# Kernel optimization log

Measured on AMD Instinct MI355X. Metric: run time of the kernel, lower is better.

Reference implementation:

```python
import jax, jax.numpy as jnp
import numpy as np

NEG = -1e9  # stands in for -inf in masked_fill; identical softmax output, grad-safe


def _sfu(inputs, fusion, Wr, Wg):
    # SFU: m = [x, f, x*f, x-f]; o = relu(m@Wr)*g + (1-g)*x, g = sigmoid(m@Wg)
    m = jnp.concatenate([inputs, fusion, inputs * fusion, inputs - fusion], axis=-1)
    x = jax.nn.relu(m @ Wr)
    g = jax.nn.sigmoid(m @ Wg)
    return x * g + (1.0 - g) * inputs


def _stage(U, V, cmask, qmask, E, B, p):
    # One Aligner stage = InterAlign followed by SelfAlign. Batch-first layout (b, len, d).
    Wu, bu, Wv, bv, Wri, Wgi, gi, W1, b1, W2, b2, Wrs, Wgs, gs = p
    # ---- InterAlign ----
    Ct = jax.nn.relu(U @ Wu + bu)              # (b, c, d)
    Qt = jax.nn.relu(V @ Wv + bv)              # (b, q, d)
    E0 = jnp.einsum('bcd,bqd->bcq', Ct, Qt)    # (b, c, q)
    if E is not None:
        Es = jax.nn.softmax(jnp.where(cmask[:, :, None] == 0, NEG, E), axis=1)   # softmax over c
        Bs = jax.nn.softmax(jnp.where(cmask[:, None, :] == 0, NEG, B), axis=2)   # softmax over c (cols)
        E = E0 + gi * jnp.einsum('bce,beq->bcq', Bs, Es)
    else:
        E = E0
    Ett = jax.nn.softmax(jnp.where(qmask[:, None, :] == 0, NEG, E), axis=2)
    qctx = jnp.einsum('bcq,bqd->bcd', Ett, V)  # attend question
    h = _sfu(U, qctx, Wri, Wgi)
    # ---- SelfAlign ----
    H1 = jax.nn.relu(h @ W1 + b1)
    H2 = jax.nn.relu(h @ W2 + b2)
    B0 = jnp.einsum('bcd,bed->bce', H1, H2)    # (b, c, c)
    if B is not None:
        B1s = jax.nn.softmax(jnp.where(cmask[:, :, None] == 0, NEG, B), axis=1)
        B2s = jax.nn.softmax(jnp.where(cmask[:, None, :] == 0, NEG, B), axis=2)
        B = B0 + gs * jnp.einsum('bce,bef->bcf', B2s, B1s)
    else:
        B = B0
    c = U.shape[1]
    B = B * (1.0 - jnp.eye(c, dtype=B.dtype))[None]  # masked_fill_(eye, 0.0): zero diagonal
    Btt = jax.nn.softmax(jnp.where(cmask[:, None, :] == 0, NEG, B), axis=2)
    hctx = jnp.einsum('bce,bed->bcd', Btt, h)
    Z = _sfu(h, hctx, Wrs, Wgs)
    return Z, E, B


def setup_inputs() -> dict:
    key = jax.random.key(0)
    b, c_len, q_len, d = 8, 768, 96, 768
    T = 2  # number of aligner stages
    ks = jax.random.split(key, 16)
    s = 0.02
    inp = {
        'U': jax.random.normal(ks[0], (b, c_len, d), jnp.float32),
        'V': jax.random.normal(ks[1], (b, q_len, d), jnp.float32),
        'U_mask': jax.random.randint(ks[2], (b, c_len), 0, 2).astype(jnp.int32),
        'V_mask': jax.random.randint(ks[3], (b, q_len), 0, 2).astype(jnp.int32),
        'Wu': jax.random.normal(ks[4], (T, d, d), jnp.float32) * s,
        'bu': jnp.zeros((T, d), jnp.float32),
        'Wv': jax.random.normal(ks[5], (T, d, d), jnp.float32) * s,
        'bv': jnp.zeros((T, d), jnp.float32),
        'Wr_i': jax.random.normal(ks[6], (T, 4 * d, d), jnp.float32) * s,
        'Wg_i': jax.random.normal(ks[7], (T, 4 * d, d), jnp.float32) * s,
        'gamma_i': jnp.full((T,), 3.0, jnp.float32),
        'W1': jax.random.normal(ks[8], (T, d, d), jnp.float32) * s,
        'b1': jnp.zeros((T, d), jnp.float32),
        'W2': jax.random.normal(ks[9], (T, d, d), jnp.float32) * s,
        'b2': jnp.zeros((T, d), jnp.float32),
        'Wr_s': jax.random.normal(ks[10], (T, 4 * d, d), jnp.float32) * s,
        'Wg_s': jax.random.normal(ks[11], (T, 4 * d, d), jnp.float32) * s,
        'gamma_s': jnp.full((T,), 3.0, jnp.float32),
    }
    return inp


def reference(U, V, U_mask, V_mask, Wu, bu, Wv, bv, Wr_i, Wg_i, gamma_i,
              W1, b1, W2, b2, Wr_s, Wg_s, gamma_s):
    E = None
    B = None
    x = U
    for t in range(Wu.shape[0]):  # fixed small stage loop (align_1 -> align_2)
        p = (Wu[t], bu[t], Wv[t], bv[t], Wr_i[t], Wg_i[t], gamma_i[t],
             W1[t], b1[t], W2[t], b2[t], Wr_s[t], Wg_s[t], gamma_s[t])
        x, E, B = _stage(x, V, U_mask, V_mask, E, B, p)
    return x
```

## Files before the change

### kernel.cpp

```cpp
#include <hip/hip_runtime.h>
#include <math.h>

#define NEGV -1e9f

typedef short bf16x8 __attribute__((ext_vector_type(8)));
typedef float f32x4 __attribute__((ext_vector_type(4)));
typedef unsigned short ushort8v __attribute__((ext_vector_type(8)));

static __device__ __forceinline__ unsigned short f2bf(float f) {
  unsigned int u = __float_as_uint(f);
  unsigned int r = (u + 0x7fffu + ((u >> 16) & 1u)) >> 16;
  return (unsigned short)r;
}

static __device__ __forceinline__ int xcd_swz(int lin, int nwg) {
  int q = nwg >> 3, r = nwg & 7;
  int x = lin & 7, i = lin >> 3;
  return (x < r) ? x * (q + 1) + i : r * (q + 1) + (x - r) * q + i;
}

__device__ __forceinline__ float wred_max(float v) {
  #pragma unroll
  for (int o = 32; o > 0; o >>= 1) v = fmaxf(v, __shfl_down(v, o, 64));
  return v;
}
__device__ __forceinline__ float wred_sum(float v) {
  #pragma unroll
  for (int o = 32; o > 0; o >>= 1) v += __shfl_down(v, o, 64);
  return v;
}

__global__ __launch_bounds__(256)
void softmax_row_mask(const float* __restrict__ X, const int* __restrict__ mask,
                      float* __restrict__ Y, unsigned short* __restrict__ Ybf,
                      int R, int Cn)
{
  int bz = blockIdx.y, r = blockIdx.x, tid = threadIdx.x;
  const float* xr = X + ((size_t)bz * R + r) * Cn;
  const int*   mr = mask + (size_t)bz * Cn;
  float*       yr = Y ? (Y + ((size_t)bz * R + r) * Cn) : nullptr;
  unsigned short* yb = Ybf ? (Ybf + ((size_t)bz * R + r) * Cn) : nullptr;
  __shared__ float sred[4];

  float mx = -INFINITY;
  for (int i = tid; i < Cn; i += 256) {
    float v = (mr[i] != 0) ? xr[i] : NEGV;
    mx = fmaxf(mx, v);
  }
  float wm = wred_max(mx);
  if ((tid & 63) == 0) sred[tid >> 6] = wm;
  __syncthreads();
  mx = fmaxf(fmaxf(sred[0], sred[1]), fmaxf(sred[2], sred[3]));
  __syncthreads();

  float s = 0.f;
  for (int i = tid; i < Cn; i += 256) {
    float v = (mr[i] != 0) ? xr[i] : NEGV;
    s += expf(v - mx);
  }
  float wsv = wred_sum(s);
  if ((tid & 63) == 0) sred[tid >> 6] = wsv;
  __syncthreads();
  s = sred[0] + sred[1] + sred[2] + sred[3];
  float inv = 1.0f / s;

// ... 143 lines not shown
  int tr = t >> 4, tc4 = (t & 15) * 4;
  #pragma unroll
  for (int rr = 0; rr < 4; ++rr) {
    int r = tr + rr * 16;
    ushort4 v = *reinterpret_cast<const ushort4*>(X + (size_t)(r0 + r) * 768 + c0 + tc4);
    T[r][tc4 + 0] = v.x; T[r][tc4 + 1] = v.y;
    T[r][tc4 + 2] = v.z; T[r][tc4 + 3] = v.w;
  }
  __syncthreads();
  #pragma unroll
  for (int rr = 0; rr < 4; ++rr) {
    int cc = tr + rr * 16;
    ushort4 o;
    o.x = T[tc4 + 0][cc]; o.y = T[tc4 + 1][cc];
    o.z = T[tc4 + 2][cc]; o.w = T[tc4 + 3][cc];
    *reinterpret_cast<ushort4*>(Y + (size_t)(c0 + cc) * 768 + r0 + tc4) = o;
  }
}

__global__ __launch_bounds__(256)
void transpV(const float* __restrict__ V, unsigned short* __restrict__ VT)
{
  int bz = blockIdx.z;
  const float* Vb = V + (size_t)bz * 96 * 768;
  unsigned short* Yb = VT + (size_t)bz * 768 * 96;
  __shared__ float T[64][65];
  int c0 = blockIdx.x * 64, r0 = blockIdx.y * 64;
  int t = threadIdx.x;
  int tr = t >> 4, tc4 = (t & 15) * 4;
  #pragma unroll
  for (int rr = 0; rr < 4; ++rr) {
    int r = tr + rr * 16;
    int gr = r0 + r;
    float4 v = make_float4(0.f, 0.f, 0.f, 0.f);
    if (gr < 96)
      v = *reinterpret_cast<const float4*>(Vb + (size_t)gr * 768 + c0 + tc4);
    T[r][tc4 + 0] = v.x; T[r][tc4 + 1] = v.y;
    T[r][tc4 + 2] = v.z; T[r][tc4 + 3] = v.w;
  }
  __syncthreads();
  #pragma unroll
  for (int rr = 0; rr < 4; ++rr) {
    int cc = tr + rr * 16;
    int gc = c0 + cc;
    #pragma unroll
    for (int e = 0; e < 4; ++e) {
      int gr = r0 + tc4 + e;
      if (gr < 96) Yb[(size_t)gc * 96 + gr] = f2bf(T[tc4 + e][cc]);
    }
  }
}

__global__ __launch_bounds__(256)
void transp_cast4(const float* __restrict__ W0, const float* __restrict__ W1a,
                  const float* __restrict__ W2a, const float* __restrict__ W3a,
                  unsigned short* __restrict__ Wt)
{
  int z = blockIdx.z;
  const float* W = (z == 0) ? W0 : (z == 1) ? W1a : (z == 2) ? W2a : W3a;
  unsigned short* Y = Wt + (size_t)z * 768 * 768;
  __shared__ float T[64][65];
  int n0 = blockIdx.x * 64, k0 = blockIdx.y * 64;
  int t = threadIdx.x;
  int tr = t >> 4, tc4 = (t & 15) * 4;
  #pragma unroll
  for (int r = 0; r < 4; ++r) {
    int k = tr + r * 16;
    float4 v = *reinterpret_cast<const float4*>(W + (size_t)(k0 + k) * 768 + n0 + tc4);
    T[k][tc4 + 0] = v.x; T[k][tc4 + 1] = v.y; T[k][tc4 + 2] = v.z; T[k][tc4 + 3] = v.w;
  }
  __syncthreads();
  #pragma unroll
  for (int r = 0; r < 4; ++r) {
    int n = tr + r * 16;
    ushort4 o;
    o.x = f2bf(T[tc4 + 0][n]); o.y = f2bf(T[tc4 + 1][n]);
    o.z = f2bf(T[tc4 + 2][n]); o.w = f2bf(T[tc4 + 3][n]);
    *reinterpret_cast<ushort4*>(Y + (size_t)(n0 + n) * 768 + k0 + tc4) = o;
  }
}

__global__ __launch_bounds__(256)
void transp_cast2x4(const float* __restrict__ W0, const float* __restrict__ W1a,
                    const float* __restrict__ W2a, const float* __restrict__ W3a,
                    unsigned short* __restrict__ Wt)
{
  int z = blockIdx.z;
  const float* W = (z == 0) ? W0 : (z == 1) ? W1a : (z == 2) ? W2a : W3a;
  unsigned short* Y = Wt + (size_t)z * 768 * 2304;
  __shared__ float T[64][65];
  int n0 = blockIdx.x * 64, k0 = blockIdx.y * 64;
  int t = threadIdx.x;
  int tr = t >> 4, tc4 = (t & 15) * 4;
  #pragma unroll
  for (int r = 0; r < 4; ++r) {
    int k = tr + r * 16;
    int gk = k0 + k;
    float4 v = *reinterpret_cast<const float4*>(W + (size_t)gk * 768 + n0 + tc4);
    if (gk < 768) {
      float4 u = *reinterpret_cast<const float4*>(W + (size_t)(gk + 2304) * 768 + n0 + tc4);
      v.x += u.x; v.y += u.y; v.z += u.z; v.w += u.w;
    } else if (gk < 1536) {
      float4 u = *reinterpret_cast<const float4*>(W + (size_t)(gk + 1536) * 768 + n0 + tc4);
      v.x -= u.x; v.y -= u.y; v.z -= u.z; v.w -= u.w;
    }
    T[k][tc4 + 0] = v.x; T[k][tc4 + 1] = v.y; T[k][tc4 + 2] = v.z; T[k][tc4 + 3] = v.w;
  }
  __syncthreads();
  #pragma unroll
  for (int r = 0; r < 4; ++r) {
    int n = tr + r * 16;
    ushort4 o;
    o.x = f2bf(T[tc4 + 0][n]); o.y = f2bf(T[tc4 + 1][n]);
    o.z = f2bf(T[tc4 + 2][n]); o.w = f2bf(T[tc4 + 3][n]);
    *reinterpret_cast<ushort4*>(Y + (size_t)(n0 + n) * 2304 + k0 + tc4) = o;
  }
}

__global__ __launch_bounds__(256)
void cast_bf16(const float* __restrict__ X, unsigned short* __restrict__ Y, int n8)
{
  int idx = blockIdx.x * 256 + threadIdx.x;
  if (idx >= n8) return;
  float4 a0 = *reinterpret_cast<const float4*>(X + (size_t)idx * 8);
  float4 a1 = *reinterpret_cast<const float4*>(X + (size_t)idx * 8 + 4);
  ushort8v o;
  o[0] = f2bf(a0.x); o[1] = f2bf(a0.y); o[2] = f2bf(a0.z); o[3] = f2bf(a0.w);
  o[4] = f2bf(a1.x); o[5] = f2bf(a1.y); o[6] = f2bf(a1.z); o[7] = f2bf(a1.w);
  *reinterpret_cast<ushort8v*>(Y + (size_t)idx * 8) = o;
}


template<int NB, int WAVES>
__global__ __launch_bounds__(64 * WAVES)
void mfma_gemm(const unsigned short* __restrict__ A,
               const unsigned short* __restrict__ Bt0,
               const unsigned short* __restrict__ Bt1,
               const float* __restrict__ bias0, const float* __restrict__ bias1,
               const float* __restrict__ alphap, const float* __restrict__ C0,
               float* __restrict__ F0, float* __restrict__ F1,
               unsigned short* __restrict__ O0, unsigned short* __restrict__ O1,
               int M, int N, int K,
               long sA, long sB, long sC0, long sC,
               int relu, int zerodiag,
               const float* __restrict__ Xc, unsigned short* __restrict__ McO)
{
  const int RG = WAVES / 4;
  const int TM = RG * 48;
  __shared__ unsigned short As[2][TM * 32];
  __shared__ unsigned short Bs0[2][2048];
  __shared__ unsigned short Bs1[2][NB == 2 ? 2048 : 16];

  int nx = gridDim.x, ny = gridDim.y;
  int nwg = nx * ny * gridDim.z;
  int lin = blockIdx.x + nx * (blockIdx.y + ny * blockIdx.z);
  int sw = xcd_swz(lin, nwg);
  int bxi = sw % nx; int rest = sw / nx;
  int byi = rest % ny; int bz = rest / ny;

  A   += (size_t)bz * sA;
  Bt0 += (size_t)bz * sB;
  if (NB == 2) Bt1 += (size_t)bz * sB;
  const float* C0b = C0 ? (C0 + (size_t)bz * sC0) : nullptr;

  int tid = threadIdx.x;
  int w = tid >> 6, l = tid & 63;
  int m0 = byi * TM, n0 = bxi * 64;
  int wr = w >> 2, wc = w & 3;

  int g8 = (((l & 3) ^ ((l >> 3) & 3))) * 8;
  int rowA = w * 16 + (l >> 2); if (rowA > TM - 1) rowA = TM - 1;
  int rB = n0 + (w & 3) * 16 + (l >> 2); if (rB > N - 1) rB = N - 1;
  const unsigned short* srcA  = A + (size_t)(m0 + rowA) * K + g8;
  const unsigned short* srcB0 = Bt0 + (size_t)rB * K + g8;
  const unsigned short* srcB1 = (NB == 2) ? Bt1 + (size_t)rB * K + g8 : nullptr;

#define GG_STAGE(kt, bi) do { int kk0 = (kt) * 32;                                                                        \
    if (w < TM / 16)                                                                                                      \
      __builtin_amdgcn_global_load_lds((const unsigned int*)(srcA + kk0),  (unsigned int*)&As[bi][0]  + w * 256, 16, 0, 0); \
    if (w < 4)                                                                                                            \
      __builtin_amdgcn_global_load_lds((const unsigned int*)(srcB0 + kk0), (unsigned int*)&Bs0[bi][0] + w * 256, 16, 0, 0); \
    if (NB == 2 && w >= 4)                                                                                                \
      __builtin_amdgcn_global_load_lds((const unsigned int*)(srcB1 + kk0), (unsigned int*)&Bs1[bi][0] + (w - 4) * 256, 16, 0, 0); \
  } while (0)

  f32x4 a0[3] = {};
  f32x4 a1v[3] = {};

  const int NT = K / 32;
  int prm = ((l >> 4) ^ ((l >> 1) & 3)) * 8;
  GG_STAGE(0, 0);
  __syncthreads();
  int cur = 0;
  for (int kt = 0; kt < NT; ++kt) {
    if (kt + 1 < NT) GG_STAGE(kt + 1, cur ^ 1);

    bf16x8 af[3];
    #pragma unroll
    for (int i = 0; i < 3; ++i) {
      int off = (wr * 48 + i * 16 + (l & 15)) * 32 + prm;
      af[i] = *reinterpret_cast<const bf16x8*>(&As[cur][off]);
    }
    int offB = (wc * 16 + (l & 15)) * 32 + prm;
    bf16x8 b0 = *reinterpret_cast<const bf16x8*>(&Bs0[cur][offB]);
    #pragma unroll
    for (int i = 0; i < 3; ++i)
      a0[i] = __builtin_amdgcn_mfma_f32_16x16x32_bf16(af[i], b0, a0[i], 0, 0, 0);
    if (NB == 2) {
      bf16x8 b1 = *reinterpret_cast<const bf16x8*>(&Bs1[cur][offB]);
      #pragma unroll
      for (int i = 0; i < 3; ++i)
        a1v[i] = __builtin_amdgcn_mfma_f32_16x16x32_bf16(af[i], b1, a1v[i], 0, 0, 0);
    }
    __syncthreads();
    cur ^= 1;
  }
#undef GG_STAGE

  float alpha = alphap ? alphap[0] : 1.0f;
  float* F0b = F0 ? F0 + (size_t)bz * sC : nullptr;
  float* F1b = F1 ? F1 + (size_t)bz * sC : nullptr;
  unsigned short* O0b = O0 ? O0 + (size_t)bz * sC : nullptr;
  unsigned short* O1b = O1 ? O1 + (size_t)bz * sC : nullptr;
  const float* Xcb = Xc ? Xc + (size_t)bz * 589824 : nullptr;
  unsigned short* Mcb = McO ? McO + (size_t)bz * 1769472 : nullptr;

  #pragma unroll
  for (int i = 0; i < 3; ++i) {
    #pragma unroll
    for (int qq = 0; qq < 4; ++qq) {
      int gm = m0 + wr * 48 + i * 16 + (l >> 4) * 4 + qq;
      int gn = n0 + wc * 16 + (l & 15);
      if (gn >= N) continue;
      size_t oidx = (size_t)gm * N + gn;
      float v = alpha * a0[i][qq];
      if (bias0) v += bias0[gn];
      if (relu) v = fmaxf(v, 0.f);
      if (C0b) v += C0b[oidx];
      if (zerodiag && gm == gn) v = 0.f;
      if (Mcb) {
        float xv = Xcb[(size_t)gm * 768 + gn];
        size_t mrow = (size_t)gm * 2304 + gn;
        Mcb[mrow]        = f2bf(xv);
        Mcb[mrow + 768]  = f2bf(v);
        Mcb[mrow + 1536] = f2bf(xv * v);
      }
      if (F0b) F0b[oidx] = v;
      if (O0b) O0b[oidx] = f2bf(v);
      if (NB == 2) {
        float v1 = alpha * a1v[i][qq];
        if (bias1) v1 += bias1[gn];
        if (relu) v1 = fmaxf(v1, 0.f);
        if (F1b) F1b[oidx] = v1;
        if (O1b) O1b[oidx] = f2bf(v1);
      }
    }
  }
}

__global__ __launch_bounds__(512)
void mfma_relu_pair(const unsigned short* __restrict__ A1g,
                    const unsigned short* __restrict__ B1g,
                    const float* __restrict__ bias1g, unsigned short* __restrict__ O1g,
                    const unsigned short* __restrict__ A2g,
                    const unsigned short* __restrict__ B2g,
                    const float* __restrict__ bias2g, unsigned short* __restrict__ O2g)
{
  const int K = 768, N = 768, NT = 24;
  __shared__ unsigned short As[2][3072];
  __shared__ unsigned short Bs0[2][2048];

  int nx = gridDim.x, ny = gridDim.y;
  int nwg = nx * ny;
  int lin = blockIdx.x + nx * blockIdx.y;
  int sw = xcd_swz(lin, nwg);
  int bxi = sw % nx; int byi = sw / nx;

  const unsigned short* A; const unsigned short* Bt;
  const float* bias; unsigned short* O;
  int m0;
  if (byi < 64) { A = A1g; Bt = B1g; bias = bias1g; O = O1g; m0 = byi * 96; }
  else          { A = A2g; Bt = B2g; bias = bias2g; O = O2g; m0 = (byi - 64) * 96; }

  int tid = threadIdx.x;
  int w = tid >> 6, l = tid & 63;
  int n0 = bxi * 64;
  int wr = w >> 2, wc = w & 3;

  int g8 = (((l & 3) ^ ((l >> 3) & 3))) * 8;
  int rowA = w * 16 + (l >> 2); if (rowA > 95) rowA = 95;
  int rB = n0 + (w & 3) * 16 + (l >> 2);
  const unsigned short* srcA  = A + (size_t)(m0 + rowA) * K + g8;
  const unsigned short* srcB0 = Bt + (size_t)rB * K + g8;

#define RP_STAGE(kt, bi) do { int kk0 = (kt) * 32;                                                                        \
    if (w < 6)                                                                                                            \
      __builtin_amdgcn_global_load_lds((const unsigned int*)(srcA + kk0),  (unsigned int*)&As[bi][0]  + w * 256, 16, 0, 0); \
    if (w < 4)                                                                                                            \
      __builtin_amdgcn_global_load_lds((const unsigned int*)(srcB0 + kk0), (unsigned int*)&Bs0[bi][0] + w * 256, 16, 0, 0); \
  } while (0)

  f32x4 a0[3] = {};
  int prm = ((l >> 4) ^ ((l >> 1) & 3)) * 8;
  RP_STAGE(0, 0);
  __syncthreads();
  int cur = 0;
  for (int kt = 0; kt < NT; ++kt) {
    if (kt + 1 < NT) RP_STAGE(kt + 1, cur ^ 1);

    bf16x8 af[3];
    #pragma unroll
    for (int i = 0; i < 3; ++i) {
      int off = (wr * 48 + i * 16 + (l & 15)) * 32 + prm;
      af[i] = *reinterpret_cast<const bf16x8*>(&As[cur][off]);
    }
    int offB = (wc * 16 + (l & 15)) * 32 + prm;
    bf16x8 b0 = *reinterpret_cast<const bf16x8*>(&Bs0[cur][offB]);
    #pragma unroll
    for (int i = 0; i < 3; ++i)
      a0[i] = __builtin_amdgcn_mfma_f32_16x16x32_bf16(af[i], b0, a0[i], 0, 0, 0);
    __syncthreads();
    cur ^= 1;
  }
#undef RP_STAGE

  #pragma unroll
  for (int i = 0; i < 3; ++i) {
    #pragma unroll
    for (int qq = 0; qq < 4; ++qq) {
      int gm = m0 + wr * 48 + i * 16 + (l >> 4) * 4 + qq;
      int gn = n0 + wc * 16 + (l & 15);
      float v = a0[i][qq] + bias[gn];
      v = fmaxf(v, 0.f);
      O[(size_t)gm * N + gn] = f2bf(v);
    }
  }
}

__global__ __launch_bounds__(512)
void qctx_fused(const float* __restrict__ E, const int* __restrict__ Vm,
                const unsigned short* __restrict__ VTb,
                const float* __restrict__ X, unsigned short* __restrict__ Mc)
{
  __shared__ unsigned short As3[3][3072];
  __shared__ unsigned short Bs3[3][2048];
  __shared__ int mk[96];

  int nx = gridDim.x, ny = gridDim.y;
  int nwg = nx * ny * gridDim.z;
  int lin = blockIdx.x + nx * (blockIdx.y + ny * blockIdx.z);
  int sw = xcd_swz(lin, nwg);
  int bxi = sw % nx; int rest = sw / nx;
  int byi = rest % ny; int bz = rest / ny;

  int tid = threadIdx.x;
  int w = tid >> 6, l = tid & 63;
  int m0 = byi * 96, n0 = bxi * 64;

  int g8 = (((l & 3) ^ ((l >> 3) & 3))) * 8;
  if (w < 4) {
    int rB = n0 + w * 16 + (l >> 2);
    const unsigned short* srcB = VTb + ((size_t)bz * 768 + rB) * 96 + g8;
    #pragma unroll
    for (int kt = 0; kt < 3; ++kt)
      __builtin_amdgcn_global_load_lds((const unsigned int*)(srcB + kt * 32),
                                       (unsigned int*)&Bs3[kt][0] + w * 256, 16, 0, 0);
  }
  if (tid < 96) mk[tid] = Vm[bz * 96 + tid];
  __syncthreads();

  if (tid < 384) {
    int r = tid >> 2, j4 = tid & 3;
    const float* er = E + ((size_t)bz * 768 + m0 + r) * 96 + j4 * 24;
    float va[24];
    #pragma unroll
    for (int u = 0; u < 6; ++u) {
      float4 v = *reinterpret_cast<const float4*>(er + u * 4);
      int kb = j4 * 24 + u * 4;
      va[u * 4 + 0] = mk[kb + 0] ? v.x : NEGV;
      va[u * 4 + 1] = mk[kb + 1] ? v.y : NEGV;
      va[u * 4 + 2] = mk[kb + 2] ? v.z : NEGV;
      va[u * 4 + 3] = mk[kb + 3] ? v.w : NEGV;
    }
    float mx = -INFINITY;
    #pragma unroll
    for (int u = 0; u < 24; ++u) mx = fmaxf(mx, va[u]);
    mx = fmaxf(mx, __shfl_xor(mx, 1, 64));
    mx = fmaxf(mx, __shfl_xor(mx, 2, 64));
    float s = 0.f;
    #pragma unroll
    for (int u = 0; u < 24; ++u) { va[u] = expf(va[u] - mx); s += va[u]; }
    s += __shfl_xor(s, 1, 64);
    s += __shfl_xor(s, 2, 64);
    float inv = 1.0f / s;
    #pragma unroll
    for (int g = 0; g < 3; ++g) {
      int gG = j4 * 3 + g;
      int kt = gG >> 2, Gin = gG & 3;
      ushort8v o;
      #pragma unroll
      for (int e = 0; e < 8; ++e) o[e] = f2bf(va[g * 8 + e] * inv);
      int idx = (r >> 4) * 512 + ((r & 15) * 4 + (Gin ^ ((r >> 1) & 3))) * 8;
      *reinterpret_cast<ushort8v*>(&As3[kt][idx]) = o;
    }
  }
  __syncthreads();

  int wr = w >> 2, wc = w & 3;
  int prm = ((l >> 4) ^ ((l >> 1) & 3)) * 8;
  f32x4 acc[3] = {};
  #pragma unroll
  for (int kt = 0; kt < 3; ++kt) {
    bf16x8 af[3];
    #pragma unroll
    for (int i = 0; i < 3; ++i) {
      int off = (wr * 48 + i * 16 + (l & 15)) * 32 + prm;
      af[i] = *reinterpret_cast<const bf16x8*>(&As3[kt][off]);
    }
    int offB = (wc * 16 + (l & 15)) * 32 + prm;
    bf16x8 b0 = *reinterpret_cast<const bf16x8*>(&Bs3[kt][offB]);
    #pragma unroll
    for (int i = 0; i < 3; ++i)
      acc[i] = __builtin_amdgcn_mfma_f32_16x16x32_bf16(af[i], b0, acc[i], 0, 0, 0);
  }

  const float* Xb = X + (size_t)bz * 589824;
  unsigned short* Mcb = Mc + (size_t)bz * 1769472;
  #pragma unroll
  for (int i = 0; i < 3; ++i) {
    #pragma unroll
    for (int qq = 0; qq < 4; ++qq) {
      int gm = m0 + wr * 48 + i * 16 + (l >> 4) * 4 + qq;
      int gn = n0 + wc * 16 + (l & 15);
      float v = acc[i][qq];
      float xv = Xb[(size_t)gm * 768 + gn];
      size_t mrow = (size_t)gm * 2304 + gn;
      Mcb[mrow]        = f2bf(xv);
      Mcb[mrow + 768]  = f2bf(v);
      Mcb[mrow + 1536] = f2bf(xv * v);
    }
  }
}

__global__ __launch_bounds__(512)
void mfma_dual2(const unsigned short* __restrict__ A1,
                const unsigned short* __restrict__ B1t,
                const unsigned short* __restrict__ A2,
                const unsigned short* __restrict__ B2t,
                const float* __restrict__ alphap, float* __restrict__ F0,
                int M, int N, int K,
                long sA1, long sB1, long sA2, long sB2, long sC,
                int zerodiag)
{
  __shared__ unsigned short As1[2][3072], Bs1[2][2048];
  __shared__ unsigned short As2[2][3072], Bs2[2][2048];

  int nx = gridDim.x, ny = gridDim.y;
  int nwg = nx * ny * gridDim.z;
  int lin = blockIdx.x + nx * (blockIdx.y + ny * blockIdx.z);
  int sw = xcd_swz(lin, nwg);
  int bxi = sw % nx; int rest = sw / nx;
  int byi = rest % ny; int bz = rest / ny;

  A1  += (size_t)bz * sA1;
  B1t += (size_t)bz * sB1;
  A2  += (size_t)bz * sA2;
  B2t += (size_t)bz * sB2;

  int tid = threadIdx.x;
  int w = tid >> 6, l = tid & 63;
  int m0 = byi * 96, n0 = bxi * 64;
  int wr = w >> 2, wc = w & 3;

  int g8 = (((l & 3) ^ ((l >> 3) & 3))) * 8;
  int rowA = w * 16 + (l >> 2); if (rowA > 95) rowA = 95;
  int rB = n0 + (w & 3) * 16 + (l >> 2);
  const unsigned short* srcA1 = A1 + (size_t)(m0 + rowA) * K + g8;
  const unsigned short* srcA2 = A2 + (size_t)(m0 + rowA) * K + g8;
  const unsigned short* srcB1 = B1t + (size_t)rB * K + g8;
  const unsigned short* srcB2 = B2t + (size_t)rB * K + g8;

#define D2_STAGE(kt, bi) do { int kk0 = (kt) * 32;                                                                        \
    if (w < 6) {                                                                                                          \
      __builtin_amdgcn_global_load_lds((const unsigned int*)(srcA1 + kk0), (unsigned int*)&As1[bi][0] + w * 256, 16, 0, 0); \
      __builtin_amdgcn_global_load_lds((const unsigned int*)(srcA2 + kk0), (unsigned int*)&As2[bi][0] + w * 256, 16, 0, 0); \
    }                                                                                                                     \
    if (w < 4)                                                                                                            \
      __builtin_amdgcn_global_load_lds((const unsigned int*)(srcB1 + kk0), (unsigned int*)&Bs1[bi][0] + w * 256, 16, 0, 0); \
    else                                                                                                                  \
      __builtin_amdgcn_global_load_lds((const unsigned int*)(srcB2 + kk0), (unsigned int*)&Bs2[bi][0] + (w - 4) * 256, 16, 0, 0); \
  } while (0)

  f32x4 ac1[3] = {};
  f32x4 ac2[3] = {};

  const int NT = K / 32;
  int prm = ((l >> 4) ^ ((l >> 1) & 3)) * 8;
  D2_STAGE(0, 0);
  __syncthreads();
  int cur = 0;
  for (int kt = 0; kt < NT; ++kt) {
    if (kt + 1 < NT) D2_STAGE(kt + 1, cur ^ 1);

    int offB = (wc * 16 + (l & 15)) * 32 + prm;
    bf16x8 af1[3], af2[3];
    #pragma unroll
    for (int i = 0; i < 3; ++i) {
      int off = (wr * 48 + i * 16 + (l & 15)) * 32 + prm;
      af1[i] = *reinterpret_cast<const bf16x8*>(&As1[cur][off]);
      af2[i] = *reinterpret_cast<const bf16x8*>(&As2[cur][off]);
    }
    bf16x8 b1 = *reinterpret_cast<const bf16x8*>(&Bs1[cur][offB]);
    bf16x8 b2 = *reinterpret_cast<const bf16x8*>(&Bs2[cur][offB]);
    #pragma unroll
    for (int i = 0; i < 3; ++i) {
      ac1[i] = __builtin_amdgcn_mfma_f32_16x16x32_bf16(af1[i], b1, ac1[i], 0, 0, 0);
      ac2[i] = __builtin_amdgcn_mfma_f32_16x16x32_bf16(af2[i], b2, ac2[i], 0, 0, 0);
    }
    __syncthreads();
    cur ^= 1;
  }
#undef D2_STAGE

  float alpha = alphap[0];
  float* F0b = F0 + (size_t)bz * sC;
  #pragma unroll
  for (int i = 0; i < 3; ++i) {
    #pragma unroll
    for (int qq = 0; qq < 4; ++qq) {
      int gm = m0 + wr * 48 + i * 16 + (l >> 4) * 4 + qq;
      int gn = n0 + wc * 16 + (l & 15);
      float v = ac1[i][qq] + alpha * ac2[i][qq];
      if (zerodiag && gm == gn) v = 0.f;
      F0b[(size_t)gm * N + gn] = v;
    }
  }
}

__global__ __launch_bounds__(512)
void sfu_mfma(const unsigned short* __restrict__ Mc,
              const unsigned short* __restrict__ Brt,
              const unsigned short* __restrict__ Bgt,
              const float* __restrict__ Xres, float* __restrict__ Z,
              unsigned short* __restrict__ Zb)
{
  __shared__ unsigned short As[2][3072];
  __shared__ unsigned short Brs[2][2048];
  __shared__ unsigned short Bgs[2][2048];
  const int K = 2304;
  const int NT = 72;

  int nx = gridDim.x, ny = gridDim.y;
  int nwg = nx * ny;
  int lin = blockIdx.x + nx * blockIdx.y;
  int sw = xcd_swz(lin, nwg);
  int bxi = sw % nx; int byi = sw / nx;

  int tid = threadIdx.x;
  int w = tid >> 6, l = tid & 63;
  int m0 = byi * 96, n0 = bxi * 64;
  int wr = w >> 2, wc = w & 3;

  int g8 = (((l & 3) ^ ((l >> 3) & 3))) * 8;
  int rowA = w * 16 + (l >> 2); if (rowA > 95) rowA = 95;
  int rB = n0 + (w & 3) * 16 + (l >> 2);
  const unsigned short* srcA = Mc  + (size_t)(m0 + rowA) * K + g8;
  const unsigned short* srcR = Brt + (size_t)rB * K + g8;
  const unsigned short* srcG = Bgt + (size_t)rB * K + g8;

#define SFU_STAGE(kt, bi) do { int kk0 = (kt) * 32;                                                                      \
    if (w < 6)                                                                                                           \
      __builtin_amdgcn_global_load_lds((const unsigned int*)(srcA + kk0), (unsigned int*)&As[bi][0]  + w * 256, 16, 0, 0); \
    if (w < 4)                                                                                                           \
      __builtin_amdgcn_global_load_lds((const unsigned int*)(srcR + kk0), (unsigned int*)&Brs[bi][0] + w * 256, 16, 0, 0); \
    if (w >= 4)                                                                                                          \
      __builtin_amdgcn_global_load_lds((const unsigned int*)(srcG + kk0), (unsigned int*)&Bgs[bi][0] + (w - 4) * 256, 16, 0, 0); \
  } while (0)

  f32x4 aR[3] = {};
  f32x4 aG[3] = {};

  int prm = ((l >> 4) ^ ((l >> 1) & 3)) * 8;
  SFU_STAGE(0, 0);
  __syncthreads();
  int cur = 0;
  for (int kt = 0; kt < NT; ++kt) {
    if (kt + 1 < NT) SFU_STAGE(kt + 1, cur ^ 1);

    bf16x8 af[3];
    #pragma unroll
    for (int i = 0; i < 3; ++i) {
      int off = (wr * 48 + i * 16 + (l & 15)) * 32 + prm;
      af[i] = *reinterpret_cast<const bf16x8*>(&As[cur][off]);
    }
    int offB = (wc * 16 + (l & 15)) * 32 + prm;
    bf16x8 br = *reinterpret_cast<const bf16x8*>(&Brs[cur][offB]);
    bf16x8 bg = *reinterpret_cast<const bf16x8*>(&Bgs[cur][offB]);
    #pragma unroll
    for (int i = 0; i < 3; ++i) {
      aR[i] = __builtin_amdgcn_mfma_f32_16x16x32_bf16(af[i], br, aR[i], 0, 0, 0);
      aG[i] = __builtin_amdgcn_mfma_f32_16x16x32_bf16(af[i], bg, aG[i], 0, 0, 0);
    }
    __syncthreads();
    cur ^= 1;
  }
#undef SFU_STAGE

  #pragma unroll
  for (int i = 0; i < 3; ++i) {
    #pragma unroll
    for (int qq = 0; qq < 4; ++qq) {
      int gm = m0 + wr * 48 + i * 16 + (l >> 4) * 4 + qq;
      int gn = n0 + wc * 16 + (l & 15);
      float r = fmaxf(aR[i][qq], 0.f);
      float g = 1.0f / (1.0f + expf(-aG[i][qq]));
      float xv = Xres[(size_t)gm * 768 + gn];
      float z = r * g + (1.0f - g) * xv;
      Z[(size_t)gm * 768 + gn] = z;
      if (Zb) Zb[(size_t)gm * 768 + gn] = f2bf(z);
    }
  }
}

static void launch_mfma1(const unsigned short* A, const unsigned short* Bt,
                         const float* bias, const float* alphap, const float* C0,
                         float* F0, unsigned short* O0,
                         int M, int N, int K, long sA, long sB, long sC0, long sC,
                         int relu, int zd, int batch, int tm, hipStream_t s,
                         const float* xcat = nullptr, unsigned short* mco = nullptr)
{
  dim3 g((N + 63) / 64, M / tm, batch);
  if (tm == 48)
    mfma_gemm<1, 4><<<g, 256, 0, s>>>(A, Bt, nullptr, bias, nullptr, alphap, C0,
                                      F0, nullptr, O0, nullptr, M, N, K, sA, sB, sC0, sC, relu, zd,
                                      xcat, mco);
  else
    mfma_gemm<1, 8><<<g, 512, 0, s>>>(A, Bt, nullptr, bias, nullptr, alphap, C0,
                                      F0, nullptr, O0, nullptr, M, N, K, sA, sB, sC0, sC, relu, zd,
                                      xcat, mco);
}

static void launch_mfma2(const unsigned short* A, const unsigned short* Bt0,
                         const unsigned short* Bt1, const float* bias0, const float* bias1,
                         unsigned short* O0, unsigned short* O1,
                         int M, int N, int K, long sA, long sB,
                         int relu, int batch, hipStream_t s)
{
  dim3 g((N + 63) / 64, M / 96, batch);
  mfma_gemm<2, 8><<<g, 512, 0, s>>>(A, Bt0, Bt1, bias0, bias1, nullptr, nullptr,
                                    nullptr, nullptr, O0, O1, M, N, K, sA, sB, 0, sA,
                                    relu, 0, nullptr, nullptr);
}

extern "C" void kernel_launch(void* const* d_in, const int* in_sizes, int n_in,
                              void* d_out, int out_size, void* d_ws, size_t ws_size,
                              hipStream_t stream)
{
  const int b = 8, c = 768, q = 96, d = 768, T = 2;
  const float* U   = (const float*)d_in[0];
  const float* V   = (const float*)d_in[1];
  const int*   Um  = (const int*)d_in[2];
  const int*   Vm  = (const int*)d_in[3];
  const float* Wu  = (const float*)d_in[4];
  const float* bu  = (const float*)d_in[5];
  const float* Wv  = (const float*)d_in[6];
  const float* bv  = (const float*)d_in[7];
  const float* Wri = (const float*)d_in[8];
  const float* Wgi = (const float*)d_in[9];
  const float* gi  = (const float*)d_in[10];
  const float* W1  = (const float*)d_in[11];
  const float* b1  = (const float*)d_in[12];
  const float* W2  = (const float*)d_in[13];
  const float* b2  = (const float*)d_in[14];
  const float* Wrs = (const float*)d_in[15];
  const float* Wgs = (const float*)d_in[16];
  const float* gs  = (const float*)d_in[17];
  float* out = (float*)d_out;

  const size_t big = (size_t)b * c * d;
  const size_t smE = (size_t)b * c * q;
  float* ws   = (float*)d_ws;
  float* xbuf = ws + 0 * big;
  float* h    = ws + 1 * big;
  float* Bm   = ws + 2 * big;
  float* t1   = ws + 3 * big;
  float* t2   = ws + 4 * big;
  float* t3   = ws + 5 * big;
  float* t4   = ws + 6 * big;
  float* Ebuf = ws + 7 * big;
  float* E0b  = Ebuf + smE;
  float* Esb  = E0b + smE;
  float* spare = Esb + smE;
  float* slotE = spare + smE;
  float* WTf  = slotE + big / 2;

  unsigned short* Mc  = (unsigned short*)t1;
  unsigned short* Wt  = (unsigned short*)t4;
  unsigned short* t1h = (unsigned short*)t1;
  unsigned short* t3h = (unsigned short*)t3;
  unsigned short* t3h2 = t3h + big;
  unsigned short* slotEb = (unsigned short*)slotE;
  unsigned short* H1b = t1h;
  unsigned short* H2b = H1b + big;
  float* SMst = spare;
  float* SSst = spare + 73728;
  unsigned short* WuT = (unsigned short*)WTf;
  unsigned short* WvT  = WuT  + (size_t)d * d;
  unsigned short* W1T  = WvT  + (size_t)d * d;
  unsigned short* W2T  = W1T  + (size_t)d * d;
  unsigned short* Vb16 = W2T  + (size_t)d * d;
  unsigned short* Qtbb = Vb16 + smE;
  unsigned short* VTb  = Qtbb + smE;
  unsigned short* EsTb = VTb  + smE;

  const long cd = (long)c * d, cq = (long)c * q, qd = (long)q * d, cc = (long)c * c;
  const size_t dd = (size_t)d * d;
  const size_t wslice = (size_t)768 * 2304;
  const int cast_big = (int)(big / 8);
  (void)ws_size;

  const float* x = U;
  for (int t = 0; t < T; ++t) {
    const float* Writ = Wri + (size_t)t * 4 * dd;
    const float* Wgit = Wgi + (size_t)t * 4 * dd;
    const float* Wrst = Wrs + (size_t)t * 4 * dd;
    const float* Wgst = Wgs + (size_t)t * 4 * dd;

    transp_cast4<<<dim3(12, 12, 4), 256, 0, stream>>>(Wu + t * dd, Wv + t * dd,
                                                      W1 + t * dd, W2 + t * dd, WuT);
    transp_cast2x4<<<dim3(12, 36, 4), 256, 0, stream>>>(Writ, Wgit, Wrst, Wgst, Wt);
    if (t == 0) {
      cast_bf16<<<dim3((int)(smE / 8 / 256)), 256, 0, stream>>>(V, Vb16, (int)(smE / 8));
      transpV<<<dim3(12, 2, b), 256, 0, stream>>>(V, VTb);
      cast_bf16<<<dim3(cast_big / 256), 256, 0, stream>>>(x, t3h, cast_big);
    }

    mfma_relu_pair<<<dim3(12, 72), 512, 0, stream>>>(t3h, WuT, bu + t * d, t1h,
                                                     Vb16, WvT, bv + t * d, Qtbb);
    float* e0dst = (t == 0) ? Ebuf : E0b;
    launch_mfma1(t1h, Qtbb, nullptr, nullptr, nullptr, e0dst, nullptr,
                 c, q, d, cd, qd, 0, cq, 0, 0, b, 48, stream);
    if (t > 0) {
      transp_f32<<<dim3(2, 12, b), 256, 0, stream>>>(Ebuf, Esb, c, q, cq, cq);
      softmax_row_mask<<<dim3(q, b), 256, 0, stream>>>(Esb, Um, nullptr, EsTb, q, c);
      launch_mfma1(t3h2, EsTb, nullptr, gi + t, E0b, Ebuf, nullptr,
                   c, q, c, cc, cq, cq, cq, 0, 0, b, 48, stream);
    }
    qctx_fused<<<dim3(12, 8, b), 512, 0, stream>>>(Ebuf, Vm, VTb, x, Mc);
    sfu_mfma<<<dim3(12, 64), 512, 0, stream>>>(Mc, Wt, Wt + wslice, x, h, t3h);
    launch_mfma2(t3h, W1T, W2T, b1 + t * d, b2 + t * d, H1b, H2b,
                 b * c, d, d, 0, 0, 1, 1, stream);
    if (t == 0) {
      launch_mfma1(H1b, H2b, nullptr, nullptr, nullptr, Bm, nullptr,
                   c, c, d, cd, cd, 0, cc, 0, 1, b, 96, stream);
    } else {
      colsm_stats<<<dim3(12, 12, b), 256, 0, stream>>>(Bm, Um, SMst, SSst, c);
      colsm_emit<<<dim3(12, 12, b), 256, 0, stream>>>(Bm, Um, SMst, SSst, slotEb, c);
      mfma_dual2<<<dim3(12, 8, b), 512, 0, stream>>>(H1b, H2b, t3h2, slotEb,
                                                     gs + t, Bm,
                                                     c, c, d, cd, cd, cc, cc, cc, 1);
    }
    softmax_row_mask<<<dim3(c, b), 256, 0, stream>>>(Bm, Um, nullptr, t3h2, c, c);
    transp_bf16<<<dim3(12, 12, b), 256, 0, stream>>>(t3h, slotEb);
    launch_mfma1(t3h2, slotEb, nullptr, nullptr, nullptr, nullptr, nullptr,
                 c, d, c, cc, cd, 0, cd, 0, 0, b, 96, stream, h, Mc);
    float* zdst = (t == T - 1) ? out : xbuf;
    unsigned short* zb16 = (t == T - 1) ? nullptr : t3h;
    sfu_mfma<<<dim3(12, 64), 512, 0, stream>>>(Mc, Wt + 2 * wslice, Wt + 3 * wslice,
                                               h, zdst, zb16);

    x = xbuf;
  }
}
```

Measured before the change: 650.6 us.

## Merge weight prep kernels, fuse E0 and gated E GEMMs, reuse bf16 residuals

Merges the two weight transpose/cast kernels into one launch. Replaces the separate E0 GEMM and gated Bs·Es GEMM with a single dual-accumulator kernel, so the E0 intermediate is never written to or read from memory. The concat builders now read the already-cast bf16 copy of x/h instead of fp32, which halves that read and skips a conversion. sfu_mfma moves from 8 to 4 waves, each covering 96 rows with six accumulators, which raises per-wave register use and may lower occupancy.

```diff
diff --git a/kernel.cpp b/kernel.cpp
--- a/kernel.cpp
+++ b/kernel.cpp
@@ -11,6 +11,9 @@
   unsigned int u = __float_as_uint(f);
   unsigned int r = (u + 0x7fffu + ((u >> 16) & 1u)) >> 16;
   return (unsigned short)r;
+}
+static __device__ __forceinline__ float bf2f(unsigned short u) {
+  return __uint_as_float((unsigned int)u << 16);
 }
 
 static __device__ __forceinline__ int xcd_swz(int lin, int nwg) {
@@ -260,68 +263,64 @@
 }
 
 __global__ __launch_bounds__(256)
-void transp_cast4(const float* __restrict__ W0, const float* __restrict__ W1a,
-                  const float* __restrict__ W2a, const float* __restrict__ W3a,
-                  unsigned short* __restrict__ Wt)
+void wprep(const float* __restrict__ S0, const float* __restrict__ S1,
+           const float* __restrict__ S2, const float* __restrict__ S3,
+           const float* __restrict__ W0, const float* __restrict__ W1a,
+           const float* __restrict__ W2a, const float* __restrict__ W3a,
+           unsigned short* __restrict__ Wt, unsigned short* __restrict__ WuT)
 {
   int z = blockIdx.z;
-  const float* W = (z == 0) ? W0 : (z == 1) ? W1a : (z == 2) ? W2a : W3a;
-  unsigned short* Y = Wt + (size_t)z * 768 * 768;
   __shared__ float T[64][65];
-  int n0 = blockIdx.x * 64, k0 = blockIdx.y * 64;
+  int n0 = blockIdx.x * 64;
   int t = threadIdx.x;
   int tr = t >> 4, tc4 = (t & 15) * 4;
-  #pragma unroll
-  for (int r = 0; r < 4; ++r) {
-    int k = tr + r * 16;
-    float4 v = *reinterpret_cast<const float4*>(W + (size_t)(k0 + k) * 768 + n0 + tc4);
-    T[k][tc4 + 0] = v.x; T[k][tc4 + 1] = v.y; T[k][tc4 + 2] = v.z; T[k][tc4 + 3] = v.w;
-  }
-  __syncthreads();
-  #pragma unroll
-  for (int r = 0; r < 4; ++r) {
-    int n = tr + r * 16;
-    ushort4 o;
-    o.x = f2bf(T[tc4 + 0][n]); o.y = f2bf(T[tc4 + 1][n]);
-    o.z = f2bf(T[tc4 + 2][n]); o.w = f2bf(T[tc4 + 3][n]);
-    *reinterpret_cast<ushort4*>(Y + (size_t)(n0 + n) * 768 + k0 + tc4) = o;
-  }
-}
-
-__global__ __launch_bounds__(256)
-void transp_cast2x4(const float* __restrict__ W0, const float* __restrict__ W1a,
-                    const float* __restrict__ W2a, const float* __restrict__ W3a,
-                    unsigned short* __restrict__ Wt)
-{
-  int z = blockIdx.z;
-  const float* W = (z == 0) ? W0 : (z == 1) ? W1a : (z == 2) ? W2a : W3a;
-  unsigned short* Y = Wt + (size_t)z * 768 * 2304;
-  __shared__ float T[64][65];
-  int n0 = blockIdx.x * 64, k0 = blockIdx.y * 64;
-  int t = threadIdx.x;
-  int tr = t >> 4, tc4 = (t & 15) * 4;
-  #pragma unroll
-  for (int r = 0; r < 4; ++r) {
-    int k = tr + r * 16;
-    int gk = k0 + k;
-    float4 v = *reinterpret_cast<const float4*>(W + (size_t)gk * 768 + n0 + tc4);
-    if (gk < 768) {
-      float4 u = *reinterpret_cast<const float4*>(W + (size_t)(gk + 2304) * 768 + n0 + tc4);
-      v.x += u.x; v.y += u.y; v.z += u.z; v.w += u.w;
-    } else if (gk < 1536) {
-      float4 u = *reinterpret_cast<const float4*>(W + (size_t)(gk + 1536) * 768 + n0 + tc4);
-      v.x -= u.x; v.y -= u.y; v.z -= u.z; v.w -= u.w;
-    }
-    T[k][tc4 + 0] = v.x; T[k][tc4 + 1] = v.y; T[k][tc4 + 2] = v.z; T[k][tc4 + 3] = v.w;
-  }
-  __syncthreads();
-  #pragma unroll
-  for (int r = 0; r < 4; ++r) {
-    int n = tr + r * 16;
-    ushort4 o;
-    o.x = f2bf(T[tc4 + 0][n]); o.y = f2bf(T[tc4 + 1][n]);
-    o.z = f2bf(T[tc4 + 2][n]); o.w = f2bf(T[tc4 + 3][n]);
-    *reinterpret_cast<ushort4*>(Y + (size_t)(n0 + n) * 2304 + k0 + tc4) = o;
+
+  if (blockIdx.y < 36) {
+    const float* W = (z == 0) ? S0 : (z == 1) ? S1 : (z == 2) ? S2 : S3;
+    unsigned short* Y = Wt + (size_t)z * 768 * 2304;
+    int k0 = blockIdx.y * 64;
+    #pragma unroll
+    for (int r = 0; r < 4; ++r) {
+      int k = tr + r * 16;
+      int gk = k0 + k;
+      float4 v = *reinterpret_cast<const float4*>(W + (size_t)gk * 768 + n0 + tc4);
+      if (gk < 768) {
+        float4 u = *reinterpret_cast<const float4*>(W + (size_t)(gk + 2304) * 768 + n0 + tc4);
+        v.x += u.x; v.y += u.y; v.z += u.z; v.w += u.w;
+      } else if (gk < 1536) {
+        float4 u = *reinterpret_cast<const float4*>(W + (size_t)(gk + 1536) * 768 + n0 + tc4);
+        v.x -= u.x; v.y -= u.y; v.z -= u.z; v.w -= u.w;
+      }
+      T[k][tc4 + 0] = v.x; T[k][tc4 + 1] = v.y; T[k][tc4 + 2] = v.z; T[k][tc4 + 3] = v.w;
+    }
+    __syncthreads();
+    #pragma unroll
+    for (int r = 0; r < 4; ++r) {
+      int n = tr + r * 16;
+      ushort4 o;
+      o.x = f2bf(T[tc4 + 0][n]); o.y = f2bf(T[tc4 + 1][n]);
+      o.z = f2bf(T[tc4 + 2][n]); o.w = f2bf(T[tc4 + 3][n]);
+      *reinterpret_cast<ushort4*>(Y + (size_t)(n0 + n) * 2304 + k0 + tc4) = o;
+    }
+  } else {
+    const float* W = (z == 0) ? W0 : (z == 1) ? W1a : (z == 2) ? W2a : W3a;
+    unsigned short* Y = WuT + (size_t)z * 768 * 768;
+    int k0 = (blockIdx.y - 36) * 64;
+    #pragma unroll
+    for (int r = 0; r < 4; ++r) {
+      int k = tr + r * 16;
+      float4 v = *reinterpret_cast<const float4*>(W + (size_t)(k0 + k) * 768 + n0 + tc4);
+      T[k][tc4 + 0] = v.x; T[k][tc4 + 1] = v.y; T[k][tc4 + 2] = v.z; T[k][tc4 + 3] = v.w;
+    }
+    __syncthreads();
+    #pragma unroll
+    for (int r = 0; r < 4; ++r) {
+      int n = tr + r * 16;
+      ushort4 o;
+      o.x = f2bf(T[tc4 + 0][n]); o.y = f2bf(T[tc4 + 1][n]);
+      o.z = f2bf(T[tc4 + 2][n]); o.w = f2bf(T[tc4 + 3][n]);
+      *reinterpret_cast<ushort4*>(Y + (size_t)(n0 + n) * 768 + k0 + tc4) = o;
+    }
   }
 }
 
@@ -351,7 +350,7 @@
                int M, int N, int K,
                long sA, long sB, long sC0, long sC,
                int relu, int zerodiag,
-               const float* __restrict__ Xc, unsigned short* __restrict__ McO)
+               const unsigned short* __restrict__ Xc, unsigned short* __restrict__ McO)
 {
   const int RG = WAVES / 4;
   const int TM = RG * 48;
@@ -430,7 +429,7 @@
   float* F1b = F1 ? F1 + (size_t)bz * sC : nullptr;
   unsigned short* O0b = O0 ? O0 + (size_t)bz * sC : nullptr;
   unsigned short* O1b = O1 ? O1 + (size_t)bz * sC : nullptr;
-  const float* Xcb = Xc ? Xc + (size_t)bz * 589824 : nullptr;
+  const unsigned short* Xcb = Xc ? Xc + (size_t)bz * 589824 : nullptr;
   unsigned short* Mcb = McO ? McO + (size_t)bz * 1769472 : nullptr;
 
   #pragma unroll
@@ -447,9 +446,10 @@
       if (C0b) v += C0b[oidx];
       if (zerodiag && gm == gn) v = 0.f;
       if (Mcb) {
-        float xv = Xcb[(size_t)gm * 768 + gn];
+        unsigned short xus = Xcb[(size_t)gm * 768 + gn];
+        float xv = bf2f(xus);
         size_t mrow = (size_t)gm * 2304 + gn;
-        Mcb[mrow]        = f2bf(xv);
+        Mcb[mrow]        = xus;
         Mcb[mrow + 768]  = f2bf(v);
         Mcb[mrow + 1536] = f2bf(xv * v);
       }
@@ -548,7 +548,7 @@
 __global__ __launch_bounds__(512)
 void qctx_fused(const float* __restrict__ E, const int* __restrict__ Vm,
                 const unsigned short* __restrict__ VTb,
-                const float* __restrict__ X, unsigned short* __restrict__ Mc)
+                const unsigned short* __restrict__ Xb16, unsigned short* __restrict__ Mc)
 {
   __shared__ unsigned short As3[3][3072];
   __shared__ unsigned short Bs3[3][2048];
@@ -632,7 +632,7 @@
       acc[i] = __builtin_amdgcn_mfma_f32_16x16x32_bf16(af[i], b0, acc[i], 0, 0, 0);
   }
 
-  const float* Xb = X + (size_t)bz * 589824;
+  const unsigned short* Xb = Xb16 + (size_t)bz * 589824;
   unsigned short* Mcb = Mc + (size_t)bz * 1769472;
   #pragma unroll
   for (int i = 0; i < 3; ++i) {
@@ -641,9 +641,10 @@
       int gm = m0 + wr * 48 + i * 16 + (l >> 4) * 4 + qq;
       int gn = n0 + wc * 16 + (l & 15);
       float v = acc[i][qq];
-      float xv = Xb[(size_t)gm * 768 + gn];
+      unsigned short xus = Xb[(size_t)gm * 768 + gn];
+      float xv = bf2f(xus);
       size_t mrow = (size_t)gm * 2304 + gn;
-      Mcb[mrow]        = f2bf(xv);
+      Mcb[mrow]        = xus;
       Mcb[mrow + 768]  = f2bf(v);
       Mcb[mrow + 1536] = f2bf(xv * v);
     }
@@ -745,7 +746,98 @@
   }
 }
 
-__global__ __launch_bounds__(512)
+__global__ __launch_bounds__(256)
+void mfma_dualE(const unsigned short* __restrict__ A1,
+                const unsigned short* __restrict__ B1t,
+                const unsigned short* __restrict__ A2,
+                const unsigned short* __restrict__ B2t,
+                const float* __restrict__ alphap, float* __restrict__ F0,
+                int M, int N, int K1, int K2,
+                long sA1, long sB1, long sA2, long sB2, long sC)
+{
+  __shared__ unsigned short As1[2][1536], Bs1[2][2048];
+  __shared__ unsigned short As2[2][1536], Bs2[2][2048];
+
+  int nx = gridDim.x, ny = gridDim.y;
+  int nwg = nx * ny * gridDim.z;
+  int lin = blockIdx.x + nx * (blockIdx.y + ny * blockIdx.z);
+  int sw = xcd_swz(lin, nwg);
+  int bxi = sw % nx; int rest = sw / nx;
+  int byi = rest % ny; int bz = rest / ny;
+
+  A1  += (size_t)bz * sA1;
+  B1t += (size_t)bz * sB1;
+  A2  += (size_t)bz * sA2;
+  B2t += (size_t)bz * sB2;
+
+  int tid = threadIdx.x;
+  int w = tid >> 6, l = tid & 63;
+  int m0 = byi * 48, n0 = bxi * 64;
+
+  int g8 = (((l & 3) ^ ((l >> 3) & 3))) * 8;
+  int rowA = w * 16 + (l >> 2); if (rowA > 47) rowA = 47;
+  int rB = n0 + w * 16 + (l >> 2); if (rB > N - 1) rB = N - 1;
+  const unsigned short* srcA1 = A1 + (size_t)(m0 + rowA) * K1 + g8;
+  const unsigned short* srcA2 = A2 + (size_t)(m0 + rowA) * K2 + g8;
+  const unsigned short* srcB1 = B1t + (size_t)rB * K1 + g8;
+  const unsigned short* srcB2 = B2t + (size_t)rB * K2 + g8;
+
+#define DE_STAGE(kt, bi) do { int kk0 = (kt) * 32;                                                                        \
+    if (w < 3) {                                                                                                          \
+      __builtin_amdgcn_global_load_lds((const unsigned int*)(srcA1 + kk0), (unsigned int*)&As1[bi][0] + w * 256, 16, 0, 0); \
+      __builtin_amdgcn_global_load_lds((const unsigned int*)(srcA2 + kk0), (unsigned int*)&As2[bi][0] + w * 256, 16, 0, 0); \
+    }                                                                                                                     \
+    __builtin_amdgcn_global_load_lds((const unsigned int*)(srcB1 + kk0), (unsigned int*)&Bs1[bi][0] + w * 256, 16, 0, 0);   \
+    __builtin_amdgcn_global_load_lds((const unsigned int*)(srcB2 + kk0), (unsigned int*)&Bs2[bi][0] + w * 256, 16, 0, 0);   \
+  } while (0)
+
+  f32x4 ac1[3] = {};
+  f32x4 ac2[3] = {};
+
+  const int NT = K1 / 32;
+  int prm = ((l >> 4) ^ ((l >> 1) & 3)) * 8;
+  DE_STAGE(0, 0);
+  __syncthreads();
+  int cur = 0;
+  for (int kt = 0; kt < NT; ++kt) {
+    if (kt + 1 < NT) DE_STAGE(kt + 1, cur ^ 1);
+
+    int offB = (w * 16 + (l & 15)) * 32 + prm;
+    bf16x8 af1[3], af2[3];
+    #pragma unroll
+    for (int i = 0; i < 3; ++i) {
+      int off = (i * 16 + (l & 15)) * 32 + prm;
+      af1[i] = *reinterpret_cast<const bf16x8*>(&As1[cur][off]);
+      af2[i] = *reinterpret_cast<const bf16x8*>(&As2[cur][off]);
+    }
+    bf16x8 b1 = *reinterpret_cast<const bf16x8*>(&Bs1[cur][offB]);
+    bf16x8 b2 = *reinterpret_cast<const bf16x8*>(&Bs2[cur][offB]);
+    #pragma unroll
+    for (int i = 0; i < 3; ++i) {
+      ac1[i] = __builtin_amdgcn_mfma_f32_16x16x32_bf16(af1[i], b1, ac1[i], 0, 0, 0);
+      ac2[i] = __builtin_amdgcn_mfma_f32_16x16x32_bf16(af2[i], b2, ac2[i], 0, 0, 0);
+    }
+    __syncthreads();
+    cur ^= 1;
+  }
+#undef DE_STAGE
+
+  float alpha = alphap[0];
+  float* F0b = F0 + (size_t)bz * sC;
+  #pragma unroll
+  for (int i = 0; i < 3; ++i) {
+    #pragma unroll
+    for (int qq = 0; qq < 4; ++qq) {
+      int gm = m0 + i * 16 + (l >> 4) * 4 + qq;
+      int gn = n0 + w * 16 + (l & 15);
+      if (gn >= N) continue;
+      float v = ac1[i][qq] + alpha * ac2[i][qq];
+      F0b[(size_t)gm * N + gn] = v;
+    }
+  }
+}
+
+__global__ __launch_bounds__(256)
 void sfu_mfma(const unsigned short* __restrict__ Mc,
               const unsigned short* __restrict__ Brt,
               const unsigned short* __restrict__ Bgt,
@@ -767,26 +859,27 @@
   int tid = threadIdx.x;
   int w = tid >> 6, l = tid & 63;
   int m0 = byi * 96, n0 = bxi * 64;
-  int wr = w >> 2, wc = w & 3;
 
   int g8 = (((l & 3) ^ ((l >> 3) & 3))) * 8;
-  int rowA = w * 16 + (l >> 2); if (rowA > 95) rowA = 95;
-  int rB = n0 + (w & 3) * 16 + (l >> 2);
-  const unsigned short* srcA = Mc  + (size_t)(m0 + rowA) * K + g8;
-  const unsigned short* srcR = Brt + (size_t)rB * K + g8;
-  const unsigned short* srcG = Bgt + (size_t)rB * K + g8;
+  int rowA1 = w * 16 + (l >> 2);
+  int rowA2 = 64 + w * 16 + (l >> 2);
+  if (rowA2 > 95) rowA2 = 95;
+  int rB = n0 + w * 16 + (l >> 2);
+  const unsigned short* srcA1 = Mc  + (size_t)(m0 + rowA1) * K + g8;
+  const unsigned short* srcA2 = Mc  + (size_t)(m0 + rowA2) * K + g8;
+  const unsigned short* srcR  = Brt + (size_t)rB * K + g8;
+  const unsigned short* srcG  = Bgt + (size_t)rB * K + g8;
 
 #define SFU_STAGE(kt, bi) do { int kk0 = (kt) * 32;                                                                      \
-    if (w < 6)                                                                                                           \
-      __builtin_amdgcn_global_load_lds((const unsigned int*)(srcA + kk0), (unsigned int*)&As[bi][0]  + w * 256, 16, 0, 0); \
-    if (w < 4)                                                                                                           \
-      __builtin_amdgcn_global_load_lds((const unsigned int*)(srcR + kk0), (unsigned int*)&Brs[bi][0] + w * 256, 16, 0, 0); \
-    if (w >= 4)                                                                                                          \
-      __builtin_amdgcn_global_load_lds((const unsigned int*)(srcG + kk0), (unsigned int*)&Bgs[bi][0] + (w - 4) * 256, 16, 0, 0); \
+    __builtin_amdgcn_global_load_lds((const unsigned int*)(srcA1 + kk0), (unsigned int*)&As[bi][0] + w * 256, 16, 0, 0);   \
+    if (w < 2)                                                                                                           \
+      __builtin_amdgcn_global_load_lds((const unsigned int*)(srcA2 + kk0), (unsigned int*)&As[bi][0] + 1024 + w * 256, 16, 0, 0); \
+    __builtin_amdgcn_global_load_lds((const unsigned int*)(srcR + kk0), (unsigned int*)&Brs[bi][0] + w * 256, 16, 0, 0);   \
+    __builtin_amdgcn_global_load_lds((const unsigned int*)(srcG + kk0), (unsigned int*)&Bgs[bi][0] + w * 256, 16, 0, 0);   \
   } while (0)
 
-  f32x4 aR[3] = {};
-  f32x4 aG[3] = {};
+  f32x4 aR[6] = {};
+  f32x4 aG[6] = {};
 
   int prm = ((l >> 4) ^ ((l >> 1) & 3)) * 8;
   SFU_STAGE(0, 0);
@@ -795,17 +888,17 @@
   for (int kt = 0; kt < NT; ++kt) {
     if (kt + 1 < NT) SFU_STAGE(kt + 1, cur ^ 1);
 
-    bf16x8 af[3];
-    #pragma unroll
-    for (int i = 0; i < 3; ++i) {
-      int off = (wr * 48 + i * 16 + (l & 15)) * 32 + prm;
+    bf16x8 af[6];
+    #pragma unroll
+    for (int i = 0; i < 6; ++i) {
+      int off = (i * 16 + (l & 15)) * 32 + prm;
       af[i] = *reinterpret_cast<const bf16x8*>(&As[cur][off]);
     }
-    int offB = (wc * 16 + (l & 15)) * 32 + prm;
+    int offB = (w * 16 + (l & 15)) * 32 + prm;
     bf16x8 br = *reinterpret_cast<const bf16x8*>(&Brs[cur][offB]);
     bf16x8 bg = *reinterpret_cast<const bf16x8*>(&Bgs[cur][offB]);
     #pragma unroll
-    for (int i = 0; i < 3; ++i) {
+    for (int i = 0; i < 6; ++i) {
       aR[i] = __builtin_amdgcn_mfma_f32_16x16x32_bf16(af[i], br, aR[i], 0, 0, 0);
       aG[i] = __builtin_amdgcn_mfma_f32_16x16x32_bf16(af[i], bg, aG[i], 0, 0, 0);
     }
@@ -815,11 +908,11 @@
 #undef SFU_STAGE
 
   #pragma unroll
-  for (int i = 0; i < 3; ++i) {
+  for (int i = 0; i < 6; ++i) {
     #pragma unroll
     for (int qq = 0; qq < 4; ++qq) {
-      int gm = m0 + wr * 48 + i * 16 + (l >> 4) * 4 + qq;
-      int gn = n0 + wc * 16 + (l & 15);
+      int gm = m0 + i * 16 + (l >> 4) * 4 + qq;
+      int gn = n0 + w * 16 + (l & 15);
       float r = fmaxf(aR[i][qq], 0.f);
       float g = 1.0f / (1.0f + expf(-aG[i][qq]));
       float xv = Xres[(size_t)gm * 768 + gn];
@@ -835,7 +928,7 @@
                          float* F0, unsigned short* O0,
                          int M, int N, int K, long sA, long sB, long sC0, long sC,
                          int relu, int zd, int batch, int tm, hipStream_t s,
-                         const float* xcat = nullptr, unsigned short* mco = nullptr)
+                         const unsigned short* xcat = nullptr, unsigned short* mco = nullptr)
 {
   dim3 g((N + 63) / 64, M / tm, batch);
   if (tm == 48)
@@ -925,7 +1018,7 @@
   const size_t dd = (size_t)d * d;
   const size_t wslice = (size_t)768 * 2304;
   const int cast_big = (int)(big / 8);
-  (void)ws_size;
+  (void)ws_size; (void)E0b;
 
   const float* x = U;
   for (int t = 0; t < T; ++t) {
@@ -934,9 +1027,9 @@
     const float* Wrst = Wrs + (size_t)t * 4 * dd;
     const float* Wgst = Wgs + (size_t)t * 4 * dd;
 
-    transp_cast4<<<dim3(12, 12, 4), 256, 0, stream>>>(Wu + t * dd, Wv + t * dd,
-                                                      W1 + t * dd, W2 + t * dd, WuT);
-    transp_cast2x4<<<dim3(12, 36, 4), 256, 0, stream>>>(Writ, Wgit, Wrst, Wgst, Wt);
+    wprep<<<dim3(12, 48, 4), 256, 0, stream>>>(Writ, Wgit, Wrst, Wgst,
+                                               Wu + t * dd, Wv + t * dd,
+                                               W1 + t * dd, W2 + t * dd, Wt, WuT);
     if (t == 0) {
       cast_bf16<<<dim3((int)(smE / 8 / 256)), 256, 0, stream>>>(V, Vb16, (int)(smE / 8));
       transpV<<<dim3(12, 2, b), 256, 0, stream>>>(V, VTb);
@@ -945,17 +1038,18 @@
 
     mfma_relu_pair<<<dim3(12, 72), 512, 0, stream>>>(t3h, WuT, bu + t * d, t1h,
                                                      Vb16, WvT, bv + t * d, Qtbb);
-    float* e0dst = (t == 0) ? Ebuf : E0b;
-    launch_mfma1(t1h, Qtbb, nullptr, nullptr, nullptr, e0dst, nullptr,
-                 c, q, d, cd, qd, 0, cq, 0, 0, b, 48, stream);
-    if (t > 0) {
+    if (t == 0) {
+      launch_mfma1(t1h, Qtbb, nullptr, nullptr, nullptr, Ebuf, nullptr,
+                   c, q, d, cd, qd, 0, cq, 0, 0, b, 48, stream);
+    } else {
       transp_f32<<<dim3(2, 12, b), 256, 0, stream>>>(Ebuf, Esb, c, q, cq, cq);
       softmax_row_mask<<<dim3(q, b), 256, 0, stream>>>(Esb, Um, nullptr, EsTb, q, c);
-      launch_mfma1(t3h2, EsTb, nullptr, gi + t, E0b, Ebuf, nullptr,
-                   c, q, c, cc, cq, cq, cq, 0, 0, b, 48, stream);
-    }
-    qctx_fused<<<dim3(12, 8, b), 512, 0, stream>>>(Ebuf, Vm, VTb, x, Mc);
-    sfu_mfma<<<dim3(12, 64), 512, 0, stream>>>(Mc, Wt, Wt + wslice, x, h, t3h);
+      mfma_dualE<<<dim3(2, 16, b), 256, 0, stream>>>(t1h, Qtbb, t3h2, EsTb,
+                                                     gi + t, Ebuf,
+                                                     c, q, d, c, cd, qd, cc, cq, cq);
+    }
+    qctx_fused<<<dim3(12, 8, b), 512, 0, stream>>>(Ebuf, Vm, VTb, t3h, Mc);
+    sfu_mfma<<<dim3(12, 64), 256, 0, stream>>>(Mc, Wt, Wt + wslice, x, h, t3h);
     launch_mfma2(t3h, W1T, W2T, b1 + t * d, b2 + t * d, H1b, H2b,
                  b * c, d, d, 0, 0, 1, 1, stream);
     if (t == 0) {
@@ -971,10 +1065,10 @@
     softmax_row_mask<<<dim3(c, b), 256, 0, stream>>>(Bm, Um, nullptr, t3h2, c, c);
     transp_bf16<<<dim3(12, 12, b), 256, 0, stream>>>(t3h, slotEb);
     launch_mfma1(t3h2, slotEb, nullptr, nullptr, nullptr, nullptr, nullptr,
-                 c, d, c, cc, cd, 0, cd, 0, 0, b, 96, stream, h, Mc);
+                 c, d, c, cc, cd, 0, cd, 0, 0, b, 96, stream, t3h, Mc);
     float* zdst = (t == T - 1) ? out : xbuf;
     unsigned short* zb16 = (t == T - 1) ? nullptr : t3h;
-    sfu_mfma<<<dim3(12, 64), 512, 0, stream>>>(Mc, Wt + 2 * wslice, Wt + 3 * wslice,
+    sfu_mfma<<<dim3(12, 64), 256, 0, stream>>>(Mc, Wt + 2 * wslice, Wt + 3 * wslice,
                                                h, zdst, zb16);
 
     x = xbuf;
```

Result: faster. 634.3 us (-2.5%).
